# Kernel optimization log

Measured on AMD Instinct MI355X. Metric: run time of the kernel, lower is better.

The kernel has to match this reference:

```python
import jax, jax.numpy as jnp
import numpy as np

B, T, D = 32, 512, 64   # batch, timesteps, latent dim
H, S = 64, 4096         # hidden_size, state_dim
EPS = 1e-6              # flax LayerNorm default epsilon


def _glorot(k, shape):
    lim = np.sqrt(6.0 / (shape[0] + shape[1])).astype(np.float32)
    return jax.random.uniform(k, shape, jnp.float32, -lim, lim)


def setup_inputs() -> dict:
    key = jax.random.key(0)
    ks = jax.random.split(key, 7)
    # gate order in the fused 4H axis: i, f, g, o ; flax inits f-gate bias to 1
    bh = jnp.concatenate([jnp.zeros((H,)), jnp.ones((H,)), jnp.zeros((2 * H,))]).astype(jnp.float32)
    return {
        "enc_outputs": jax.random.normal(ks[0], (B, T, D), jnp.float32),
        "Wx": _glorot(ks[1], (D, 4 * H)),   # input->gates, no bias (flax dense_i)
        "Wh": _glorot(ks[2], (H, 4 * H)),   # hidden->gates
        "bh": bh,
        "W1": _glorot(ks[3], (H, 2 * H)), "b1": jnp.zeros((2 * H,), jnp.float32),
        "g1": jnp.ones((2 * H,), jnp.float32), "be1": jnp.zeros((2 * H,), jnp.float32),
        "W2": _glorot(ks[4], (2 * H, 2 * H)), "b2": jnp.zeros((2 * H,), jnp.float32),
        "g2": jnp.ones((2 * H,), jnp.float32), "be2": jnp.zeros((2 * H,), jnp.float32),
        "Wo": _glorot(ks[5], (2 * H, S)), "bo": jnp.zeros((S,), jnp.float32),
    }


def _layernorm(x, g, b):
    m = x.mean(-1, keepdims=True)
    v = ((x - m) ** 2).mean(-1, keepdims=True)
    return (x - m) * jax.lax.rsqrt(v + EPS) * g + b


def _lstm(enc, Wx, Wh, bh):
    # precompute all input projections in one big GEMM: [B,T,4H]
    xg = jnp.einsum('btd,dg->btg', enc, Wx)

    def step(carry, x_t):
        c, h = carry
        z = x_t + h @ Wh + bh              # [B,4H]
        i, f, g, o = jnp.split(z, 4, axis=-1)
        c = jax.nn.sigmoid(f) * c + jax.nn.sigmoid(i) * jnp.tanh(g)
        h = jax.nn.sigmoid(o) * jnp.tanh(c)
        return (c, h), h

    b = enc.shape[0]
    init = (jnp.zeros((b, H), enc.dtype), jnp.zeros((b, H), enc.dtype))
    _, hs = jax.lax.scan(step, init, xg.swapaxes(0, 1))  # hs: [T,B,H]
    return hs.swapaxes(0, 1)                              # [B,T,H]


def reference(enc_outputs, Wx, Wh, bh, W1, b1, g1, be1, W2, b2, g2, be2, Wo, bo):
    b, t, _ = enc_outputs.shape
    dec = _lstm(enc_outputs, Wx, Wh, bh)            # [B,T,H]
    flat = dec.reshape(b * t, H)
    h = jax.nn.gelu(_layernorm(flat @ W1 + b1, g1, be1))   # flax gelu: tanh approx
    # dropout deterministic (train=False) -> identity
    h = jax.nn.gelu(_layernorm(h @ W2 + b2, g2, be2))
    out = h @ Wo + bo                                # [B*T,S]
    return out.reshape(b, t, S)
```

## Files before the change

### kernel.cpp

```cpp
#include <hip/hip_runtime.h>
#include <hip/hip_bf16.h>

#define T_ 512

typedef __attribute__((ext_vector_type(8))) short short8;
typedef __attribute__((ext_vector_type(4))) float f32x4;

__device__ __forceinline__ float fast_rcp(float x){ return __builtin_amdgcn_rcpf(x); }
__device__ __forceinline__ float sigmoid_f(float x){
  return fast_rcp(1.f + __expf(-x));
}
__device__ __forceinline__ float tanh_f(float x){
  return fmaf(2.f, fast_rcp(1.f + __expf(-2.f*x)), -1.f);
}
__device__ __forceinline__ float gelu_f(float x){
  float u = 0.7978845608028654f*(x + 0.044715f*x*x*x);
  return 0.5f*x*(1.f + tanh_f(u));
}
__device__ __forceinline__ float readlane_f(float v, int lane){
  return __int_as_float(__builtin_amdgcn_readlane(__float_as_int(v), lane));
}

__global__ __launch_bounds__(256, 1) void k_xg(const float* __restrict__ enc,
                                               const float* __restrict__ Wx,
                                               const float* __restrict__ bh,
                                               float* __restrict__ xg)
{
  __shared__ __align__(16) float es[64*64];
  int j = threadIdx.x;
  int g = blockIdx.x;
  const float* encg = enc + (size_t)g*64*64;
  for (int idx = j; idx < 64*64; idx += 256) es[idx] = encg[idx];
  float wx[64];
#pragma unroll
  for (int k = 0; k < 64; ++k) wx[k] = Wx[k*256 + j];
  float bj = bh[j];
  __syncthreads();
  float* xo = xg + (size_t)g*64*256;
  for (int r = 0; r < 64; ++r){
    const float4* e4 = (const float4*)(es + r*64);
    float z0 = bj, z1 = 0.f, z2 = 0.f, z3 = 0.f;
#pragma unroll
    for (int k4 = 0; k4 < 16; ++k4){
      float4 v = e4[k4];
      z0 = fmaf(v.x, wx[4*k4+0], z0);
      z1 = fmaf(v.y, wx[4*k4+1], z1);
      z2 = fmaf(v.z, wx[4*k4+2], z2);
      z3 = fmaf(v.w, wx[4*k4+3], z3);
    }
    xo[r*256 + j] = (z0+z1)+(z2+z3);
  }
}

__global__ __launch_bounds__(256, 1) void k_lstm(const float* __restrict__ xg,
                                                 const float* __restrict__ Wh,
                                                 float* __restrict__ hs)
{
  __shared__ __align__(16) float zsm[2][256];
  int tid = threadIdx.x;
  int w = tid >> 6, l = tid & 63;
  int j = tid;
  int b = blockIdx.x;
  float wh[64];
#pragma unroll
  for (int k = 0; k < 64; ++k) wh[k] = Wh[k*256 + j];
  float c = 0.f;
  const float* xr = xg + (size_t)b*T_*256;
  float* ho = hs + (size_t)b*T_*64;
  float xn0 = xr[1*256 + j];
  float xn1 = xr[2*256 + j];
  float xn2 = xr[3*256 + j];
  float xn3 = xr[4*256 + j];
  zsm[0][j] = xr[j];
  __syncthreads();

#define LSTM_STEP(tt, xn)                                                     \
  {                                                                           \
    const float* zb = zsm[(tt) & 1];                                          \
    float zi = zb[l], zf = zb[64+l], zg_ = zb[128+l], zo = zb[192+l];         \
    c = sigmoid_f(zf)*c + sigmoid_f(zi)*tanh_f(zg_);                          \
    float h = sigmoid_f(zo)*tanh_f(c);                                        \
    if (w == 0) ho[(size_t)(tt)*64 + l] = h;                                  \
    if ((tt) + 1 < T_){                                                       \
      float z0 = (xn), z1 = 0.f, z2 = 0.f, z3 = 0.f;                          \
      if ((tt) + 5 < T_) (xn) = xr[(size_t)((tt)+5)*256 + j];                 \
      _Pragma("unroll")                                                       \
      for (int k = 0; k < 64; k += 4){                                        \
        z0 = fmaf(readlane_f(h, k+0), wh[k+0], z0);                           \
        z1 = fmaf(readlane_f(h, k+1), wh[k+1], z1);                           \
        z2 = fmaf(readlane_f(h, k+2), wh[k+2], z2);                           \
        z3 = fmaf(readlane_f(h, k+3), wh[k+3], z3);                           \
      }                                                                       \
      zsm[((tt)+1) & 1][j] = (z0+z1)+(z2+z3);                                 \
    }                                                                         \
    __syncthreads();                                                          \
  }

  for (int t = 0; t < T_; t += 4){
    LSTM_STEP(t,   xn0);
    LSTM_STEP(t+1, xn1);
    LSTM_STEP(t+2, xn2);
    LSTM_STEP(t+3, xn3);
  }
#undef LSTM_STEP
}

__global__ __launch_bounds__(256, 1) void k_mlp(const float* __restrict__ hs,
    const float* __restrict__ W1, const float* __restrict__ b1,
    const float* __restrict__ g1, const float* __restrict__ be1,
    const float* __restrict__ W2, const float* __restrict__ b2,
    const float* __restrict__ g2, const float* __restrict__ be2,
    __hip_bfloat16* __restrict__ h2g)
{
  __shared__ __align__(16) float xs[2][64];
  __shared__ __align__(16) float vs[2][128];
  __shared__ float red[2][2][2];
  int tid = threadIdx.x;
  int jj = tid & 127, rg = tid >> 7;
  int lane = tid & 63;
  int whalf = (tid >> 6) & 1;
  float w1c[64], w2c[128];
#pragma unroll
  for (int k = 0; k < 64; ++k) w1c[k] = W1[k*128 + jj];
#pragma unroll
  for (int k = 0; k < 128; ++k) w2c[k] = W2[k*128 + jj];
  float b1j = b1[jj], g1j = g1[jj], be1j = be1[jj];
  float b2j = b2[jj], g2j = g2[jj], be2j = be2[jj];
  int base = blockIdx.x * 64;
  for (int p = 0; p < 32; ++p){
    int r = base + p*2 + rg;
    if (whalf == 0) xs[rg][lane] = hs[(size_t)r*64 + lane];
    __syncthreads();
    float a0 = b1j, a1 = 0.f;
    const float4* x4 = (const float4*)xs[rg];
#pragma unroll
    for (int k4 = 0; k4 < 16; ++k4){
      float4 v = x4[k4];
      a0 = fmaf(v.x, w1c[4*k4+0], a0);
      a1 = fmaf(v.y, w1c[4*k4+1], a1);
      a0 = fmaf(v.z, w1c[4*k4+2], a0);
      a1 = fmaf(v.w, w1c[4*k4+3], a1);
    }
    float a = a0 + a1;
    float s1 = a, s2 = a*a;
#pragma unroll
    for (int off = 32; off > 0; off >>= 1){
      s1 += __shfl_xor(s1, off, 64);
      s2 += __shfl_xor(s2, off, 64);
    }
    if (lane == 0){ red[rg][whalf][0] = s1; red[rg][whalf][1] = s2; }
    __syncthreads();
    s1 = red[rg][0][0] + red[rg][1][0];
    s2 = red[rg][0][1] + red[rg][1][1];
    float mean = s1*(1.f/128.f);
    float var  = s2*(1.f/128.f) - mean*mean;
    float rstd = rsqrtf(var + 1e-6f);
    float y = gelu_f((a - mean)*rstd*g1j + be1j);
    vs[rg][jj] = y;
    __syncthreads();
    float c0 = b2j, c1 = 0.f;
    const float4* v4 = (const float4*)vs[rg];
#pragma unroll
    for (int k4 = 0; k4 < 32; ++k4){
      float4 v = v4[k4];
      c0 = fmaf(v.x, w2c[4*k4+0], c0);
      c1 = fmaf(v.y, w2c[4*k4+1], c1);
      c0 = fmaf(v.z, w2c[4*k4+2], c0);
      c1 = fmaf(v.w, w2c[4*k4+3], c1);
    }
    float cc = c0 + c1;
    float t1 = cc, t2 = cc*cc;
#pragma unroll
    for (int off = 32; off > 0; off >>= 1){
      t1 += __shfl_xor(t1, off, 64);
      t2 += __shfl_xor(t2, off, 64);
    }
    if (lane == 0){ red[rg][whalf][0] = t1; red[rg][whalf][1] = t2; }
    __syncthreads();
    t1 = red[rg][0][0] + red[rg][1][0];
    t2 = red[rg][0][1] + red[rg][1][1];
    mean = t1*(1.f/128.f);
    var  = t2*(1.f/128.f) - mean*mean;
    rstd = rsqrtf(var + 1e-6f);
    float z = gelu_f((cc - mean)*rstd*g2j + be2j);
    h2g[(size_t)r*128 + jj] = __float2bfloat16(z);
  }
}

__global__ __launch_bounds__(256, 1) void k_wot(const float* __restrict__ Wo,
                                                __hip_bfloat16* __restrict__ WoT)
{
  __shared__ __hip_bfloat16 tl[64][130];
  int tid = threadIdx.x;
  int n0 = blockIdx.x * 64;
  for (int idx = tid; idx < 64*128; idx += 256){
    int k = idx >> 6, nl = idx & 63;
    tl[nl][k] = __float2bfloat16(Wo[(size_t)k*4096 + n0 + nl]);
  }
  __syncthreads();
  for (int idx = tid; idx < 64*128; idx += 256){
    int nl = idx >> 7, k = idx & 127;
    WoT[(size_t)(n0 + nl)*128 + k] = tl[nl][k];
  }
}

__global__ __launch_bounds__(256, 1) void k_out(const __hip_bfloat16* __restrict__ h2g,
                                                const __hip_bfloat16* __restrict__ WoT,
                                                const float* __restrict__ bo,
                                                float* __restrict__ out)
{
  int bid = blockIdx.x;
  int Mb = bid >> 5, Nb = bid & 31;
  int tid = threadIdx.x;
  int w = tid >> 6, l = tid & 63;
  int wm = w >> 1, wn = w & 1;
  int m0 = Mb*128 + wm*64, n0 = Nb*128 + wn*64;
  int lr = l & 15, lk = (l >> 4)*8;
  f32x4 acc[4][4] = {};
  const short* A  = (const short*)WoT;
  const short* Bp = (const short*)h2g;
#pragma unroll
  for (int kk = 0; kk < 4; ++kk){
    int ko = kk*32 + lk;
    short8 av[4], bv[4];
#pragma unroll
    for (int i = 0; i < 4; ++i) av[i] = *(const short8*)(A  + (size_t)(n0 + i*16 + lr)*128 + ko);
#pragma unroll
    for (int i = 0; i < 4; ++i) bv[i] = *(const short8*)(Bp + (size_t)(m0 + i*16 + lr)*128 + ko);
#pragma unroll
    for (int fm = 0; fm < 4; ++fm)
#pragma unroll
      for (int fn = 0; fn < 4; ++fn)
        acc[fm][fn] = __builtin_amdgcn_mfma_f32_16x16x32_bf16(av[fn], bv[fm], acc[fm][fn], 0, 0, 0);
  }
  int nb_ = (l >> 4)*4;
#pragma unroll
  for (int fn = 0; fn < 4; ++fn){
    f32x4 bia = *(const f32x4*)(bo + n0 + fn*16 + nb_);
#pragma unroll
    for (int fm = 0; fm < 4; ++fm){
      size_t row = (size_t)(m0 + fm*16 + lr)*4096;
      __builtin_nontemporal_store(acc[fm][fn] + bia, (f32x4*)(out + row + n0 + fn*16 + nb_));
    }
  }
}

extern "C" void kernel_launch(void* const* d_in, const int* in_sizes, int n_in,
                              void* d_out, int out_size, void* d_ws, size_t ws_size,
                              hipStream_t stream)
{
  const float* enc = (const float*)d_in[0];
  const float* Wx  = (const float*)d_in[1];
  const float* Wh  = (const float*)d_in[2];
  const float* bh  = (const float*)d_in[3];
  const float* W1  = (const float*)d_in[4];
  const float* b1  = (const float*)d_in[5];
  const float* g1  = (const float*)d_in[6];
  const float* be1 = (const float*)d_in[7];
  const float* W2  = (const float*)d_in[8];
  const float* b2  = (const float*)d_in[9];
  const float* g2  = (const float*)d_in[10];
  const float* be2 = (const float*)d_in[11];
  const float* Wo  = (const float*)d_in[12];
  const float* bo  = (const float*)d_in[13];
  float* out = (float*)d_out;

  const size_t xg_bytes = (size_t)16384*256*4;
  const size_t hs_bytes = (size_t)16384*64*4;
  const size_t h2_bytes = (size_t)16384*128*2;
  const size_t wt_bytes = (size_t)4096*128*2;
  char* ws = (char*)d_ws;
  float *xg, *hs; __hip_bfloat16 *h2g, *WoT;
  if (ws_size >= xg_bytes + hs_bytes + h2_bytes + wt_bytes){
    xg  = (float*)ws;
    hs  = (float*)(ws + xg_bytes);
    h2g = (__hip_bfloat16*)(ws + xg_bytes + hs_bytes);
    WoT = (__hip_bfloat16*)(ws + xg_bytes + hs_bytes + h2_bytes);
  } else {
    xg  = (float*)d_out;
    hs  = (float*)((char*)d_out + xg_bytes);
    h2g = (__hip_bfloat16*)ws;
    WoT = (__hip_bfloat16*)(ws + h2_bytes);
  }

  k_xg  <<<256,  256, 0, stream>>>(enc, Wx, bh, xg);
  k_wot <<<64,   256, 0, stream>>>(Wo, WoT);
  k_lstm<<<32,   256, 0, stream>>>(xg, Wh, hs);
  k_mlp <<<256,  256, 0, stream>>>(hs, W1, b1, g1, be1, W2, b2, g2, be2, h2g);
  k_out <<<4096, 256, 0, stream>>>(h2g, WoT, bo, out);
}
```

Measured before the change: 426.0 us.

## Compute LSTM recurrence with bf16 MFMA, batching 16 sequences per block

The LSTM kernel now computes the hidden-to-gate product with bf16 MFMA 16x16x32 instructions. Each block handles 16 batch rows, so 2 blocks replace the previous 32, and the hidden state is exchanged through shared memory as bf16. A new kernel transposes Wh to bf16 ahead of time. The aim is to replace the serial readlane/FMA chain per step with a few matrix instructions, at the cost of less parallelism across CUs and reduced precision in the recurrent state. Launch-bound minimum-block hints are also dropped on the other kernels.

```diff
diff --git a/kernel.cpp b/kernel.cpp
--- a/kernel.cpp
+++ b/kernel.cpp
@@ -17,14 +17,15 @@
   float u = 0.7978845608028654f*(x + 0.044715f*x*x*x);
   return 0.5f*x*(1.f + tanh_f(u));
 }
-__device__ __forceinline__ float readlane_f(float v, int lane){
-  return __int_as_float(__builtin_amdgcn_readlane(__float_as_int(v), lane));
-}
-
-__global__ __launch_bounds__(256, 1) void k_xg(const float* __restrict__ enc,
-                                               const float* __restrict__ Wx,
-                                               const float* __restrict__ bh,
-                                               float* __restrict__ xg)
+__device__ __forceinline__ unsigned short bf16_bits(float x){
+  __hip_bfloat16 b = __float2bfloat16(x);
+  return __builtin_bit_cast(unsigned short, b);
+}
+
+__global__ __launch_bounds__(256) void k_xg(const float* __restrict__ enc,
+                                            const float* __restrict__ Wx,
+                                            const float* __restrict__ bh,
+                                            float* __restrict__ xg)
 {
   __shared__ __align__(16) float es[64*64];
   int j = threadIdx.x;
@@ -52,60 +53,92 @@
   }
 }
 
+__global__ __launch_bounds__(256) void k_whT(const float* __restrict__ Wh,
+                                             __hip_bfloat16* __restrict__ WhT)
+{
+  int idx = blockIdx.x*256 + threadIdx.x;
+  int k = idx >> 8, j = idx & 255;
+  WhT[j*64 + k] = __float2bfloat16(Wh[idx]);
+}
+
 __global__ __launch_bounds__(256, 1) void k_lstm(const float* __restrict__ xg,
-                                                 const float* __restrict__ Wh,
+                                                 const __hip_bfloat16* __restrict__ WhT,
                                                  float* __restrict__ hs)
 {
-  __shared__ __align__(16) float zsm[2][256];
+  __shared__ __align__(16) __hip_bfloat16 Hb[2][16][72];
   int tid = threadIdx.x;
   int w = tid >> 6, l = tid & 63;
-  int j = tid;
-  int b = blockIdx.x;
-  float wh[64];
-#pragma unroll
-  for (int k = 0; k < 64; ++k) wh[k] = Wh[k*256 + j];
-  float c = 0.f;
-  const float* xr = xg + (size_t)b*T_*256;
-  float* ho = hs + (size_t)b*T_*64;
-  float xn0 = xr[1*256 + j];
-  float xn1 = xr[2*256 + j];
-  float xn2 = xr[3*256 + j];
-  float xn3 = xr[4*256 + j];
-  zsm[0][j] = xr[j];
+  int m = l & 15;
+  int q = l >> 4;
+  int bo = blockIdx.x * 16;
+  int col0 = 16*w + 4*q;
+
+  short8 av[4][2];
+#pragma unroll
+  for (int g = 0; g < 4; ++g)
+#pragma unroll
+    for (int kk = 0; kk < 2; ++kk)
+      av[g][kk] = *(const short8*)((const short*)WhT + (64*g + 16*w + m)*64 + kk*32 + q*8);
+
+  for (int i = tid; i < 1152; i += 256) ((unsigned int*)&Hb[0][0][0])[i] = 0;
+
+  float c0 = 0.f, c1 = 0.f, c2 = 0.f, c3 = 0.f;
+  const float* xrow = xg + (size_t)(bo + m)*T_*256;
+  float* horow = hs + (size_t)(bo + m)*T_*64;
+  f32x4 xa[4], xb[4];
+#pragma unroll
+  for (int g = 0; g < 4; ++g) xa[g] = *(const f32x4*)(xrow + 0*256 + 64*g + col0);
+#pragma unroll
+  for (int g = 0; g < 4; ++g) xb[g] = *(const f32x4*)(xrow + 1*256 + 64*g + col0);
   __syncthreads();
 
-#define LSTM_STEP(tt, xn)                                                     \
-  {                                                                           \
-    const float* zb = zsm[(tt) & 1];                                          \
-    float zi = zb[l], zf = zb[64+l], zg_ = zb[128+l], zo = zb[192+l];         \
-    c = sigmoid_f(zf)*c + sigmoid_f(zi)*tanh_f(zg_);                          \
-    float h = sigmoid_f(zo)*tanh_f(c);                                        \
-    if (w == 0) ho[(size_t)(tt)*64 + l] = h;                                  \
-    if ((tt) + 1 < T_){                                                       \
-      float z0 = (xn), z1 = 0.f, z2 = 0.f, z3 = 0.f;                          \
-      if ((tt) + 5 < T_) (xn) = xr[(size_t)((tt)+5)*256 + j];                 \
-      _Pragma("unroll")                                                       \
-      for (int k = 0; k < 64; k += 4){                                        \
-        z0 = fmaf(readlane_f(h, k+0), wh[k+0], z0);                           \
-        z1 = fmaf(readlane_f(h, k+1), wh[k+1], z1);                           \
-        z2 = fmaf(readlane_f(h, k+2), wh[k+2], z2);                           \
-        z3 = fmaf(readlane_f(h, k+3), wh[k+3], z3);                           \
-      }                                                                       \
-      zsm[((tt)+1) & 1][j] = (z0+z1)+(z2+z3);                                 \
-    }                                                                         \
-    __syncthreads();                                                          \
-  }
-
-  for (int t = 0; t < T_; t += 4){
-    LSTM_STEP(t,   xn0);
-    LSTM_STEP(t+1, xn1);
-    LSTM_STEP(t+2, xn2);
-    LSTM_STEP(t+3, xn3);
-  }
-#undef LSTM_STEP
-}
-
-__global__ __launch_bounds__(256, 1) void k_mlp(const float* __restrict__ hs,
+#define STEP(tt, X)                                                            \
+  {                                                                            \
+    const short* hbase = (const short*)&Hb[(tt) & 1][0][0];                    \
+    short8 bv0 = *(const short8*)(hbase + m*72 + q*8);                         \
+    short8 bv1 = *(const short8*)(hbase + m*72 + 32 + q*8);                    \
+    f32x4 z0 = __builtin_amdgcn_mfma_f32_16x16x32_bf16(av[0][0], bv0, X[0], 0,0,0); \
+    f32x4 z1 = __builtin_amdgcn_mfma_f32_16x16x32_bf16(av[1][0], bv0, X[1], 0,0,0); \
+    f32x4 z2 = __builtin_amdgcn_mfma_f32_16x16x32_bf16(av[2][0], bv0, X[2], 0,0,0); \
+    f32x4 z3 = __builtin_amdgcn_mfma_f32_16x16x32_bf16(av[3][0], bv0, X[3], 0,0,0); \
+    z0 = __builtin_amdgcn_mfma_f32_16x16x32_bf16(av[0][1], bv1, z0, 0,0,0);    \
+    z1 = __builtin_amdgcn_mfma_f32_16x16x32_bf16(av[1][1], bv1, z1, 0,0,0);    \
+    z2 = __builtin_amdgcn_mfma_f32_16x16x32_bf16(av[2][1], bv1, z2, 0,0,0);    \
+    z3 = __builtin_amdgcn_mfma_f32_16x16x32_bf16(av[3][1], bv1, z3, 0,0,0);    \
+    if ((tt) + 2 < T_){                                                        \
+      _Pragma("unroll")                                                        \
+      for (int g = 0; g < 4; ++g)                                              \
+        X[g] = *(const f32x4*)(xrow + (size_t)((tt)+2)*256 + 64*g + col0);     \
+    }                                                                          \
+    float h0, h1, h2, h3;                                                      \
+    { float zi=z0[0], zf=z1[0], zg_=z2[0], zo=z3[0];                           \
+      c0 = sigmoid_f(zf)*c0 + sigmoid_f(zi)*tanh_f(zg_);                       \
+      h0 = sigmoid_f(zo)*tanh_f(c0); }                                         \
+    { float zi=z0[1], zf=z1[1], zg_=z2[1], zo=z3[1];                           \
+      c1 = sigmoid_f(zf)*c1 + sigmoid_f(zi)*tanh_f(zg_);                       \
+      h1 = sigmoid_f(zo)*tanh_f(c1); }                                         \
+    { float zi=z0[2], zf=z1[2], zg_=z2[2], zo=z3[2];                           \
+      c2 = sigmoid_f(zf)*c2 + sigmoid_f(zi)*tanh_f(zg_);                       \
+      h2 = sigmoid_f(zo)*tanh_f(c2); }                                         \
+    { float zi=z0[3], zf=z1[3], zg_=z2[3], zo=z3[3];                           \
+      c3 = sigmoid_f(zf)*c3 + sigmoid_f(zi)*tanh_f(zg_);                       \
+      h3 = sigmoid_f(zo)*tanh_f(c3); }                                         \
+    *(f32x4*)(horow + (size_t)(tt)*64 + col0) = (f32x4){h0, h1, h2, h3};       \
+    ushort4 hp;                                                                \
+    hp.x = bf16_bits(h0); hp.y = bf16_bits(h1);                                \
+    hp.z = bf16_bits(h2); hp.w = bf16_bits(h3);                                \
+    *(ushort4*)((unsigned short*)&Hb[((tt)+1) & 1][0][0] + m*72 + col0) = hp;  \
+    __syncthreads();                                                           \
+  }
+
+  for (int t = 0; t < T_; t += 2){
+    STEP(t,   xa);
+    STEP(t+1, xb);
+  }
+#undef STEP
+}
+
+__global__ __launch_bounds__(256) void k_mlp(const float* __restrict__ hs,
     const float* __restrict__ W1, const float* __restrict__ b1,
     const float* __restrict__ g1, const float* __restrict__ be1,
     const float* __restrict__ W2, const float* __restrict__ b2,
@@ -187,8 +220,8 @@
   }
 }
 
-__global__ __launch_bounds__(256, 1) void k_wot(const float* __restrict__ Wo,
-                                                __hip_bfloat16* __restrict__ WoT)
+__global__ __launch_bounds__(256) void k_wot(const float* __restrict__ Wo,
+                                             __hip_bfloat16* __restrict__ WoT)
 {
   __shared__ __hip_bfloat16 tl[64][130];
   int tid = threadIdx.x;
@@ -204,10 +237,10 @@
   }
 }
 
-__global__ __launch_bounds__(256, 1) void k_out(const __hip_bfloat16* __restrict__ h2g,
-                                                const __hip_bfloat16* __restrict__ WoT,
-                                                const float* __restrict__ bo,
-                                                float* __restrict__ out)
+__global__ __launch_bounds__(256) void k_out(const __hip_bfloat16* __restrict__ h2g,
+                                             const __hip_bfloat16* __restrict__ WoT,
+                                             const float* __restrict__ bo,
+                                             float* __restrict__ out)
 {
   int bid = blockIdx.x;
   int Mb = bid >> 5, Nb = bid & 31;
@@ -265,27 +298,31 @@
   const float* bo  = (const float*)d_in[13];
   float* out = (float*)d_out;
 
-  const size_t xg_bytes = (size_t)16384*256*4;
-  const size_t hs_bytes = (size_t)16384*64*4;
-  const size_t h2_bytes = (size_t)16384*128*2;
-  const size_t wt_bytes = (size_t)4096*128*2;
+  const size_t xg_bytes  = (size_t)16384*256*4;
+  const size_t hs_bytes  = (size_t)16384*64*4;
+  const size_t h2_bytes  = (size_t)16384*128*2;
+  const size_t wt_bytes  = (size_t)4096*128*2;
+  const size_t wht_bytes = (size_t)256*64*2;
   char* ws = (char*)d_ws;
-  float *xg, *hs; __hip_bfloat16 *h2g, *WoT;
-  if (ws_size >= xg_bytes + hs_bytes + h2_bytes + wt_bytes){
+  float *xg, *hs; __hip_bfloat16 *h2g, *WoT, *WhT;
+  if (ws_size >= xg_bytes + hs_bytes + h2_bytes + wt_bytes + wht_bytes){
     xg  = (float*)ws;
     hs  = (float*)(ws + xg_bytes);
     h2g = (__hip_bfloat16*)(ws + xg_bytes + hs_bytes);
     WoT = (__hip_bfloat16*)(ws + xg_bytes + hs_bytes + h2_bytes);
+    WhT = (__hip_bfloat16*)(ws + xg_bytes + hs_bytes + h2_bytes + wt_bytes);
   } else {
     xg  = (float*)d_out;
     hs  = (float*)((char*)d_out + xg_bytes);
     h2g = (__hip_bfloat16*)ws;
     WoT = (__hip_bfloat16*)(ws + h2_bytes);
+    WhT = (__hip_bfloat16*)(ws + h2_bytes + wt_bytes);
   }
 
   k_xg  <<<256,  256, 0, stream>>>(enc, Wx, bh, xg);
+  k_whT <<<64,   256, 0, stream>>>(Wh, WhT);
   k_wot <<<64,   256, 0, stream>>>(Wo, WoT);
-  k_lstm<<<32,   256, 0, stream>>>(xg, Wh, hs);
+  k_lstm<<<2,    256, 0, stream>>>(xg, WhT, hs);
   k_mlp <<<256,  256, 0, stream>>>(hs, W1, b1, g1, be1, W2, b2, g2, be2, h2g);
   k_out <<<4096, 256, 0, stream>>>(h2g, WoT, bo, out);
 }
```

Result: slower. 544.9 us (+27.9%).
